# Kernel optimization log

Hardware: AMD Instinct MI355X
Metric: run time of the kernel (lower is better)

The kernel has to match this reference:

```python
import jax, jax.numpy as jnp
import numpy as np

H = 8
D_MODEL = 512
D_K = D_MODEL // H
NEG = -1e9


def setup_inputs() -> dict:
    key = jax.random.key(0)
    ks = jax.random.split(key, 11)
    B, S = 2, 2048
    scale = 1.0 / np.sqrt(D_MODEL)
    inp = {
        'query': jax.random.normal(ks[0], (B, S, D_MODEL), dtype=jnp.float32),
        'key': jax.random.normal(ks[1], (B, S, D_MODEL), dtype=jnp.float32),
        'value': jax.random.normal(ks[2], (B, S, D_MODEL), dtype=jnp.float32),
        'Wq': jax.random.normal(ks[3], (D_MODEL, D_MODEL), dtype=jnp.float32) * scale,
        'bq': jnp.zeros((D_MODEL,), dtype=jnp.float32),
        'Wk': jax.random.normal(ks[4], (D_MODEL, D_MODEL), dtype=jnp.float32) * scale,
        'bk': jnp.zeros((D_MODEL,), dtype=jnp.float32),
        'Wv': jax.random.normal(ks[5], (D_MODEL, D_MODEL), dtype=jnp.float32) * scale,
        'bv': jnp.zeros((D_MODEL,), dtype=jnp.float32),
        'Wo': jax.random.normal(ks[6], (D_MODEL, D_MODEL), dtype=jnp.float32) * scale,
        'bo': jnp.zeros((D_MODEL,), dtype=jnp.float32),
    }
    return inp


def reference(query, key, value, Wq, bq, Wk, bk, Wv, bv, Wo, bo):
    B, S, _ = query.shape
    # QKV projections (nn.Linear: x @ W.T + b), split into heads -> [B, H, S, D_K]
    def proj(x, W, b):
        return (x @ W.T + b).reshape(B, S, H, D_K).transpose(0, 2, 1, 3)

    q = proj(query, Wq, bq)
    k = proj(key, Wk, bk)
    v = proj(value, Wv, bv)

    scores = jnp.einsum('bhqd,bhkd->bhqk', q, k) / jnp.sqrt(jnp.float32(D_K))
    # diagonal mask (mask=True): token cannot attend to itself
    diag = jnp.eye(S, dtype=bool)
    scores = jnp.where(diag, NEG, scores)

    p_attn = jax.nn.softmax(scores, axis=-1)  # [B, H, S, S]
    x = jnp.einsum('bhqk,bhkd->bhqd', p_attn, v)
    x = x.transpose(0, 2, 1, 3).reshape(B, S, H * D_K)
    return x @ Wo.T + bo
```

## Files before the change

### kernel.cpp

```cpp
#include <hip/hip_runtime.h>
#include <hip/hip_bf16.h>
#include <math.h>

#define NUM_H 8
#define DK    64
#define DM    512
#define SEQ   2048
#define NB    2
#define MROWS (NB*SEQ)

typedef unsigned short u16;
typedef unsigned int   u32;
typedef __attribute__((ext_vector_type(8))) __bf16 bf16x8;
typedef __attribute__((ext_vector_type(4))) float  f32x4;

__device__ __forceinline__ u16 f2bf(float v) {
    union { float f; u32 i; } x; x.f = v;
    u32 r = (x.i + 0x7FFFu + ((x.i >> 16) & 1u)) >> 16;
    return (u16)r;
}
__device__ __forceinline__ u16 f2h(float v) {
    union { _Float16 h; u16 u; } x; x.h = (_Float16)v; return x.u;
}
__device__ __forceinline__ float h2f(u16 u) {
    union { u16 u; _Float16 h; } x; x.u = u; return (float)x.h;
}
__device__ __forceinline__ bf16x8 ld_bf8(const u16* p) {
    union { uint4 u; bf16x8 v; } t;
    t.u = *(const uint4*)p;
    return t.v;
}
__device__ __forceinline__ uint4 pack8bf(const float* f) {
    uint4 o;
    o.x = (u32)f2bf(f[0]) | ((u32)f2bf(f[1]) << 16);
    o.y = (u32)f2bf(f[2]) | ((u32)f2bf(f[3]) << 16);
    o.z = (u32)f2bf(f[4]) | ((u32)f2bf(f[5]) << 16);
    o.w = (u32)f2bf(f[6]) | ((u32)f2bf(f[7]) << 16);
    return o;
}

__global__ __launch_bounds__(256) void convAll(
    const float* __restrict__ q, const float* __restrict__ k,
    const float* __restrict__ Wq, const float* __restrict__ Wk,
    const float* __restrict__ Wv, const float* __restrict__ Wo,
    u16* __restrict__ Xqk, u16* __restrict__ Wscr)
{
    const int z = blockIdx.y;
    const float* src;
    u16* dst;
    if (z == 0)      { src = q; dst = Xqk; }
    else if (z == 1) { src = k; dst = Xqk + 2097152; }
    else {
        if (blockIdx.x >= 128) return;
        src = (z == 2) ? Wq : (z == 3) ? Wk : (z == 4) ? Wv : Wo;
        dst = Wscr + (size_t)(z - 2) * 262144;
    }
    int i = (blockIdx.x * 256 + threadIdx.x) * 8;
    float4 a = *(const float4*)(src + i);
    float4 b = *(const float4*)(src + i + 4);
    float f[8] = {a.x, a.y, a.z, a.w, b.x, b.y, b.z, b.w};
    *(uint4*)&dst[i] = pack8bf(f);
}

#define MODE_QK 0
#define MODE_VT 1
#define MODE_FIN 2

template<int MODE, bool INBF, bool WBF>
__device__ __forceinline__ void gemm_core(
    const void* __restrict__ Xv, const void* __restrict__ Wv_,
    const float* __restrict__ bias, void* __restrict__ outv,
    u16* As, u16* Bs, int row0, int col0)
{
    const int tid = threadIdx.x;
    const int lane = tid & 63, w = tid >> 6;
    const int ln15 = lane & 15, quad = lane >> 4;
    const int wm = (w >> 1) * 64, wn = (w & 1) * 32;

    f32x4 acc[4][2];
#pragma unroll
    for (int mt = 0; mt < 4; ++mt)
#pragma unroll
        for (int nt = 0; nt < 2; ++nt) acc[mt][nt] = (f32x4){0.f, 0.f, 0.f, 0.f};

    for (int kt = 0; kt < DM; kt += 64) {
        __syncthreads();
#pragma unroll
        for (int g = 0; g < 4; ++g) {
            int idx = g * 2048 + tid * 8;
            int r = idx >> 6, c = idx & 63;
            if (INBF) {
                *(uint4*)&As[r * 72 + c] =
                    *(const uint4*)((const u16*)Xv + (size_t)(row0 + r) * DM + kt + c);
            } else {
                const float* xp = (const float*)Xv + (size_t)(row0 + r) * DM + kt + c;
                float4 a = *(const float4*)xp;
                float4 b2 = *(const float4*)(xp + 4);
                float f[8] = {a.x, a.y, a.z, a.w, b2.x, b2.y, b2.z, b2.w};
                *(uint4*)&As[r * 72 + c] = pack8bf(f);
            }
        }
#pragma unroll
        for (int g = 0; g < 2; ++g) {
            int idx = g * 2048 + tid * 8;
            int r = idx >> 6, c = idx & 63;
            if (WBF) {
                *(uint4*)&Bs[r * 72 + c] =
                    *(const uint4*)((const u16*)Wv_ + (size_t)(col0 + r) * DM + kt + c);
            } else {
                const float* wp = (const float*)Wv_ + (size_t)(col0 + r) * DM + kt + c;
                float4 a = *(const float4*)wp;
                float4 b2 = *(const float4*)(wp + 4);
                float f[8] = {a.x, a.y, a.z, a.w, b2.x, b2.y, b2.z, b2.w};
                *(uint4*)&Bs[r * 72 + c] = pack8bf(f);
            }
        }
        __syncthreads();

#pragma unroll
        for (int ks = 0; ks < 2; ++ks) {
            bf16x8 af[4], bfr[2];
#pragma unroll
            for (int mt = 0; mt < 4; ++mt)
                af[mt] = ld_bf8(&As[(wm + mt * 16 + ln15) * 72 + ks * 32 + quad * 8]);
#pragma unroll
            for (int nt = 0; nt < 2; ++nt)
                bfr[nt] = ld_bf8(&Bs[(wn + nt * 16 + ln15) * 72 + ks * 32 + quad * 8]);
#pragma unroll
            for (int mt = 0; mt < 4; ++mt)
#pragma unroll
                for (int nt = 0; nt < 2; ++nt)
                    acc[mt][nt] = __builtin_amdgcn_mfma_f32_16x16x32_bf16(
                        af[mt], bfr[nt], acc[mt][nt], 0, 0, 0);
        }
    }

    float bc[2];
#pragma unroll
    for (int nt = 0; nt < 2; ++nt) bc[nt] = bias[col0 + wn + nt * 16 + ln15];
    const int h = col0 >> 6;

    if (MODE == MODE_FIN) {
        float* outF = (float*)outv;
#pragma unroll
        for (int mt = 0; mt < 4; ++mt)
#pragma unroll
            for (int r = 0; r < 4; ++r) {
                int m = row0 + wm + mt * 16 + quad * 4 + r;
#pragma unroll
                for (int nt = 0; nt < 2; ++nt)
                    outF[(size_t)m * DM + col0 + wn + nt * 16 + ln15] = acc[mt][nt][r] + bc[nt];
            }
    } else if (MODE == MODE_QK) {
        u16* outB = (u16*)outv;
#pragma unroll
        for (int mt = 0; mt < 4; ++mt)
#pragma unroll
            for (int r = 0; r < 4; ++r) {
                int m = row0 + wm + mt * 16 + quad * 4 + r;
                int b = m >> 11, s2 = m & (SEQ - 1);
#pragma unroll
                for (int nt = 0; nt < 2; ++nt) {
                    int dk = wn + nt * 16 + ln15;
                    outB[((size_t)((b * NUM_H + h) * SEQ + s2)) * DK + dk] =
                        f2bf(acc[mt][nt][r] + bc[nt]);
                }
            }
    } else {
        u16* outB = (u16*)outv;
        __syncthreads();
#pragma unroll
        for (int mt = 0; mt < 4; ++mt)
#pragma unroll
            for (int nt = 0; nt < 2; ++nt) {
                int dk = wn + nt * 16 + ln15;
#pragma unroll
                for (int r = 0; r < 4; ++r) {
                    int sl = wm + mt * 16 + quad * 4 + r;
                    As[dk * 136 + sl] = f2bf(acc[mt][nt][r] + bc[nt]);
                }
            }
        __syncthreads();
        int dk = tid >> 2, ch = (tid & 3) * 32;
        int b = row0 >> 11, s0 = row0 & (SEQ - 1);
        size_t base = ((size_t)((b * NUM_H + h) * DK + dk)) * SEQ + s0 + ch;
#pragma unroll
        for (int c4 = 0; c4 < 4; ++c4)
            *(uint4*)&outB[base + c4 * 8] = *(const uint4*)&As[dk * 136 + ch + c4 * 8];
    }
}

__global__ __launch_bounds__(256) void qkv_mfma(
    const u16* __restrict__ xq, const u16* __restrict__ xk, const float* __restrict__ xv,
    const u16* __restrict__ Wscr,
    const float* __restrict__ b0, const float* __restrict__ b1, const float* __restrict__ b2,
    u16* __restrict__ oQ, u16* __restrict__ oK, u16* __restrict__ oVt)
{
    __shared__ u16 As[128 * 72];
    __shared__ u16 Bs[64 * 72];
    const int row0 = blockIdx.x * 128, col0 = blockIdx.y * 64;
    const int z = blockIdx.z;
    const u16* W = Wscr + (size_t)z * 262144;
    if (z == 2)
        gemm_core<MODE_VT, false, true>(xv, W, b2, oVt, As, Bs, row0, col0);
    else if (z == 0)
        gemm_core<MODE_QK, true, true>(xq, W, b0, oQ, As, Bs, row0, col0);
    else
        gemm_core<MODE_QK, true, true>(xk, W, b1, oK, As, Bs, row0, col0);
}

__global__ __launch_bounds__(256) void final_mfma(
    const u16* __restrict__ X, const u16* __restrict__ Wbf,
    const float* __restrict__ bias, float* __restrict__ out)
{
    __shared__ u16 As[128 * 72];
    __shared__ u16 Bs[64 * 72];
    gemm_core<MODE_FIN, true, true>(X, Wbf, bias, out, As, Bs,
                                    blockIdx.x * 128, blockIdx.y * 64);
}

#define LSTR 72
__global__ __launch_bounds__(256) void attn_mfma(
    const u16* __restrict__ Qg, const u16* __restrict__ Kg,
    const u16* __restrict__ Vtg, u16* __restrict__ Pd, float* __restrict__ Cl)
{
    __shared__ u16 Klds[64 * LSTR];
    __shared__ u16 Vtlds[64 * LSTR];
    __shared__ u16 Pls[64 * LSTR];

    const int tid = threadIdx.x;
    const int lane = tid & 63;
    const int w = tid >> 6;
    const int ln15 = lane & 15;
    const int quad = lane >> 4;
    const int bh = blockIdx.y;
    const int b = bh >> 3, h = bh & 7;
    const int qb = blockIdx.x * 64;
    const int z = blockIdx.z;
    const int k0 = z * (SEQ / 2), k1 = k0 + SEQ / 2;

    const u16* Qp = Qg + (size_t)bh * SEQ * DK;
    const u16* Kp = Kg + (size_t)bh * SEQ * DK;
    const u16* Vp = Vtg + (size_t)bh * DK * SEQ;

    const int qrowA = qb + w * 16 + ln15;
    const bf16x8 qa0 = ld_bf8(&Qp[(size_t)qrowA * DK + quad * 8]);
    const bf16x8 qa1 = ld_bf8(&Qp[(size_t)qrowA * DK + 32 + quad * 8]);

    f32x4 O[4];
    float l_i[4] = {0.f, 0.f, 0.f, 0.f};
#pragma unroll
    for (int nt = 0; nt < 4; ++nt) O[nt] = (f32x4){0.f, 0.f, 0.f, 0.f};

    const int sr = tid >> 3;
    const int scl = (tid & 7) * 8;

    for (int kt = k0; kt < k1; kt += 64) {
        __syncthreads();
        *(uint4*)&Klds[sr * LSTR + scl]         = *(const uint4*)&Kp[(size_t)(kt + sr) * DK + scl];
        *(uint4*)&Klds[(sr + 32) * LSTR + scl]  = *(const uint4*)&Kp[(size_t)(kt + sr + 32) * DK + scl];
        *(uint4*)&Vtlds[sr * LSTR + scl]        = *(const uint4*)&Vp[(size_t)sr * SEQ + kt + scl];
        *(uint4*)&Vtlds[(sr + 32) * LSTR + scl] = *(const uint4*)&Vp[(size_t)(sr + 32) * SEQ + kt + scl];
        __syncthreads();

        const bool diagt = (kt == qb);
#pragma unroll
        for (int nt2 = 0; nt2 < 4; ++nt2) {
            bf16x8 kb0 = ld_bf8(&Klds[(nt2 * 16 + ln15) * LSTR + quad * 8]);
            bf16x8 kb1 = ld_bf8(&Klds[(nt2 * 16 + ln15) * LSTR + 32 + quad * 8]);
            f32x4 zacc = (f32x4){0.f, 0.f, 0.f, 0.f};
            zacc = __builtin_amdgcn_mfma_f32_16x16x32_bf16(qa0, kb0, zacc, 0, 0, 0);
            zacc = __builtin_amdgcn_mfma_f32_16x16x32_bf16(qa1, kb1, zacc, 0, 0, 0);
#pragma unroll
            for (int r = 0; r < 4; ++r) {
                float e = __expf(fmaf(zacc[r], 0.125f, -4.0f));
                if (diagt && (nt2 * 16 + ln15 == w * 16 + quad * 4 + r)) e = 0.f;
                l_i[r] += e;
                Pls[(w * 16 + quad * 4 + r) * LSTR + nt2 * 16 + ln15] = f2bf(e);
            }
        }

        bf16x8 pa0 = ld_bf8(&Pls[(w * 16 + ln15) * LSTR + quad * 8]);
        bf16x8 pa1 = ld_bf8(&Pls[(w * 16 + ln15) * LSTR + 32 + quad * 8]);
#pragma unroll
        for (int nt = 0; nt < 4; ++nt) {
            bf16x8 vb0 = ld_bf8(&Vtlds[(nt * 16 + ln15) * LSTR + quad * 8]);
            bf16x8 vb1 = ld_bf8(&Vtlds[(nt * 16 + ln15) * LSTR + 32 + quad * 8]);
            O[nt] = __builtin_amdgcn_mfma_f32_16x16x32_bf16(pa0, vb0, O[nt], 0, 0, 0);
            O[nt] = __builtin_amdgcn_mfma_f32_16x16x32_bf16(pa1, vb1, O[nt], 0, 0, 0);
        }
    }

#pragma unroll
    for (int r = 0; r < 4; ++r) {
        float s = l_i[r];
        s += __shfl_xor(s, 1);
        s += __shfl_xor(s, 2);
        s += __shfl_xor(s, 4);
        s += __shfl_xor(s, 8);
        l_i[r] = s;
    }
    if (ln15 == 0) {
#pragma unroll
        for (int r = 0; r < 4; ++r)
            Cl[(size_t)z * 32768 + bh * SEQ + qb + w * 16 + quad * 4 + r] = l_i[r];
    }
#pragma unroll
    for (int r = 0; r < 4; ++r) {
        int s = qb + w * 16 + quad * 4 + r;
        size_t base = (size_t)z * 2097152 + ((size_t)(b * SEQ + s)) * DM + h * DK;
#pragma unroll
        for (int nt = 0; nt < 4; ++nt)
            Pd[base + nt * 16 + ln15] = f2h(O[nt][r] * 0.015625f);
    }
}

__global__ __launch_bounds__(256) void combine(
    const u16* __restrict__ Pd, const float* __restrict__ Cl, u16* __restrict__ C)
{
    int idx = (blockIdx.x * 256 + threadIdx.x) * 8;
    int row = idx >> 9, col = idx & 511;
    int b = row >> 11, s = row & (SEQ - 1), h = col >> 6;
    int bh = b * NUM_H + h;
    float lsum = Cl[bh * SEQ + s] + Cl[32768 + bh * SEQ + s];
    float sc = 64.f / lsum;
    uint4 u0 = *(const uint4*)&Pd[idx];
    uint4 u1 = *(const uint4*)&Pd[2097152 + idx];
    u32 a0[4] = {u0.x, u0.y, u0.z, u0.w};
    u32 a1[4] = {u1.x, u1.y, u1.z, u1.w};
    float f[8];
#pragma unroll
    for (int j = 0; j < 4; ++j) {
        f[2 * j]     = (h2f((u16)(a0[j] & 0xffff)) + h2f((u16)(a1[j] & 0xffff))) * sc;
        f[2 * j + 1] = (h2f((u16)(a0[j] >> 16))    + h2f((u16)(a1[j] >> 16)))    * sc;
    }
    *(uint4*)&C[idx] = pack8bf(f);
}

extern "C" void kernel_launch(void* const* d_in, const int* in_sizes, int n_in,
                              void* d_out, int out_size, void* d_ws, size_t ws_size,
                              hipStream_t stream) {
    const float* q  = (const float*)d_in[0];
    const float* k  = (const float*)d_in[1];
    const float* v  = (const float*)d_in[2];
    const float* Wq = (const float*)d_in[3];
    const float* bq = (const float*)d_in[4];
    const float* Wk = (const float*)d_in[5];
    const float* bk = (const float*)d_in[6];
    const float* Wv = (const float*)d_in[7];
    const float* bv = (const float*)d_in[8];
    const float* Wo = (const float*)d_in[9];
    const float* bo = (const float*)d_in[10];
    float* out = (float*)d_out;

    const size_t TSZ = (size_t)MROWS * DM;
    u16* Qb  = (u16*)d_ws;
    u16* Kb  = Qb + TSZ;
    u16* Vtb = Qb + 2 * TSZ;
    u16* CbU = Qb + 3 * TSZ;
    float* Cl  = (float*)CbU;
    u16*  Wscr = CbU + 131072;

    u16* Xqk = (u16*)d_out;
    u16* Pd  = (u16*)d_out;

    dim3 blk(256);
    hipLaunchKernelGGL(convAll, dim3(1024, 6), blk, 0, stream, q, k, Wq, Wk, Wv, Wo, Xqk, Wscr);
    dim3 gq(MROWS / 128, DM / 64, 3);
    hipLaunchKernelGGL(qkv_mfma, gq, blk, 0, stream,
                       Xqk, Xqk + TSZ, v, Wscr, bq, bk, bv, Qb, Kb, Vtb);
    dim3 ga(SEQ / 64, NB * NUM_H, 2);
    hipLaunchKernelGGL(attn_mfma, ga, blk, 0, stream, Qb, Kb, Vtb, Pd, Cl);
    hipLaunchKernelGGL(combine, dim3(1024), blk, 0, stream, Pd, Cl, Qb);
    dim3 gf(MROWS / 128, DM / 64);
    hipLaunchKernelGGL(final_mfma, gf, blk, 0, stream, Qb, Wscr + 3 * 262144, bo, out);
}
```

Baseline: 174.0 us.

## Double-buffer LDS tiles with register prefetch in GEMM and attention loops

Both the projection GEMM core and the attention kernel now load the next K-tile from global memory into registers while MFMAs run on the current LDS buffer. The prefetched data is then written into a second LDS buffer, which leaves one barrier per iteration instead of two. This is meant to hide global-load latency behind compute. The LDS row stride also drops from 72 to 68 elements, which changes the bank mapping but makes odd rows only 8-byte aligned for 16-byte accesses, so it may cost alignment or bank-conflict penalties. LDS footprint roughly doubles, which may reduce occupancy.

```diff
diff --git a/kernel.cpp b/kernel.cpp
--- a/kernel.cpp
+++ b/kernel.cpp
@@ -13,6 +13,10 @@
 typedef unsigned int   u32;
 typedef __attribute__((ext_vector_type(8))) __bf16 bf16x8;
 typedef __attribute__((ext_vector_type(4))) float  f32x4;
+
+#define ASTR 68
+#define ABUF (128*ASTR)
+#define BBUF (64*ASTR)
 
 __device__ __forceinline__ u16 f2bf(float v) {
     union { float f; u32 i; } x; x.f = v;
@@ -66,9 +70,9 @@
 #define MODE_VT 1
 #define MODE_FIN 2
 
-template<int MODE, bool INBF, bool WBF>
+template<int MODE, bool INBF>
 __device__ __forceinline__ void gemm_core(
-    const void* __restrict__ Xv, const void* __restrict__ Wv_,
+    const void* __restrict__ Xv, const u16* __restrict__ Wb,
     const float* __restrict__ bias, void* __restrict__ outv,
     u16* As, u16* Bs, int row0, int col0)
 {
@@ -77,55 +81,75 @@
     const int ln15 = lane & 15, quad = lane >> 4;
     const int wm = (w >> 1) * 64, wn = (w & 1) * 32;
 
+    const int rA = tid >> 3;
+    const int cA = (tid & 7) * 8;
+
     f32x4 acc[4][2];
 #pragma unroll
     for (int mt = 0; mt < 4; ++mt)
 #pragma unroll
         for (int nt = 0; nt < 2; ++nt) acc[mt][nt] = (f32x4){0.f, 0.f, 0.f, 0.f};
 
-    for (int kt = 0; kt < DM; kt += 64) {
-        __syncthreads();
-#pragma unroll
-        for (int g = 0; g < 4; ++g) {
-            int idx = g * 2048 + tid * 8;
-            int r = idx >> 6, c = idx & 63;
-            if (INBF) {
-                *(uint4*)&As[r * 72 + c] =
-                    *(const uint4*)((const u16*)Xv + (size_t)(row0 + r) * DM + kt + c);
-            } else {
-                const float* xp = (const float*)Xv + (size_t)(row0 + r) * DM + kt + c;
-                float4 a = *(const float4*)xp;
-                float4 b2 = *(const float4*)(xp + 4);
-                float f[8] = {a.x, a.y, a.z, a.w, b2.x, b2.y, b2.z, b2.w};
-                *(uint4*)&As[r * 72 + c] = pack8bf(f);
-            }
-        }
-#pragma unroll
-        for (int g = 0; g < 2; ++g) {
-            int idx = g * 2048 + tid * 8;
-            int r = idx >> 6, c = idx & 63;
-            if (WBF) {
-                *(uint4*)&Bs[r * 72 + c] =
-                    *(const uint4*)((const u16*)Wv_ + (size_t)(col0 + r) * DM + kt + c);
-            } else {
-                const float* wp = (const float*)Wv_ + (size_t)(col0 + r) * DM + kt + c;
-                float4 a = *(const float4*)wp;
-                float4 b2 = *(const float4*)(wp + 4);
-                float f[8] = {a.x, a.y, a.z, a.w, b2.x, b2.y, b2.z, b2.w};
-                *(uint4*)&Bs[r * 72 + c] = pack8bf(f);
-            }
-        }
-        __syncthreads();
-
+    uint4 aU[4];
+    float4 aF0[4], aF1[4];
+    uint4 bU[2];
+
+#pragma unroll
+    for (int g = 0; g < 4; ++g) {
+        int r = row0 + g * 32 + rA;
+        if (INBF) aU[g] = *(const uint4*)((const u16*)Xv + (size_t)r * DM + cA);
+        else {
+            const float* xp = (const float*)Xv + (size_t)r * DM + cA;
+            aF0[g] = *(const float4*)xp; aF1[g] = *(const float4*)(xp + 4);
+        }
+    }
+#pragma unroll
+    for (int g = 0; g < 2; ++g)
+        bU[g] = *(const uint4*)(Wb + (size_t)(col0 + g * 32 + rA) * DM + cA);
+
+#pragma unroll
+    for (int g = 0; g < 4; ++g) {
+        if (!INBF) {
+            float f[8] = {aF0[g].x, aF0[g].y, aF0[g].z, aF0[g].w,
+                          aF1[g].x, aF1[g].y, aF1[g].z, aF1[g].w};
+            aU[g] = pack8bf(f);
+        }
+        *(uint4*)&As[(g * 32 + rA) * ASTR + cA] = aU[g];
+    }
+#pragma unroll
+    for (int g = 0; g < 2; ++g)
+        *(uint4*)&Bs[(g * 32 + rA) * ASTR + cA] = bU[g];
+    __syncthreads();
+
+    int cur = 0;
+    for (int kt_i = 0; kt_i < 8; ++kt_i) {
+        const int ktn = (kt_i + 1) * 64;
+        if (kt_i < 7) {
+#pragma unroll
+            for (int g = 0; g < 4; ++g) {
+                int r = row0 + g * 32 + rA;
+                if (INBF) aU[g] = *(const uint4*)((const u16*)Xv + (size_t)r * DM + ktn + cA);
+                else {
+                    const float* xp = (const float*)Xv + (size_t)r * DM + ktn + cA;
+                    aF0[g] = *(const float4*)xp; aF1[g] = *(const float4*)(xp + 4);
+                }
+            }
+#pragma unroll
+            for (int g = 0; g < 2; ++g)
+                bU[g] = *(const uint4*)(Wb + (size_t)(col0 + g * 32 + rA) * DM + ktn + cA);
+        }
+
+        const u16* Ab = As + cur * ABUF;
+        const u16* Bb = Bs + cur * BBUF;
 #pragma unroll
         for (int ks = 0; ks < 2; ++ks) {
             bf16x8 af[4], bfr[2];
 #pragma unroll
             for (int mt = 0; mt < 4; ++mt)
-                af[mt] = ld_bf8(&As[(wm + mt * 16 + ln15) * 72 + ks * 32 + quad * 8]);
+                af[mt] = ld_bf8(&Ab[(wm + mt * 16 + ln15) * ASTR + ks * 32 + quad * 8]);
 #pragma unroll
             for (int nt = 0; nt < 2; ++nt)
-                bfr[nt] = ld_bf8(&Bs[(wn + nt * 16 + ln15) * 72 + ks * 32 + quad * 8]);
+                bfr[nt] = ld_bf8(&Bb[(wn + nt * 16 + ln15) * ASTR + ks * 32 + quad * 8]);
 #pragma unroll
             for (int mt = 0; mt < 4; ++mt)
 #pragma unroll
@@ -133,6 +157,25 @@
                     acc[mt][nt] = __builtin_amdgcn_mfma_f32_16x16x32_bf16(
                         af[mt], bfr[nt], acc[mt][nt], 0, 0, 0);
         }
+
+        if (kt_i < 7) {
+            u16* An = As + (1 - cur) * ABUF;
+            u16* Bn = Bs + (1 - cur) * BBUF;
+#pragma unroll
+            for (int g = 0; g < 4; ++g) {
+                if (!INBF) {
+                    float f[8] = {aF0[g].x, aF0[g].y, aF0[g].z, aF0[g].w,
+                                  aF1[g].x, aF1[g].y, aF1[g].z, aF1[g].w};
+                    aU[g] = pack8bf(f);
+                }
+                *(uint4*)&An[(g * 32 + rA) * ASTR + cA] = aU[g];
+            }
+#pragma unroll
+            for (int g = 0; g < 2; ++g)
+                *(uint4*)&Bn[(g * 32 + rA) * ASTR + cA] = bU[g];
+        }
+        __syncthreads();
+        cur ^= 1;
     }
 
     float bc[2];
@@ -168,7 +211,6 @@
             }
     } else {
         u16* outB = (u16*)outv;
-        __syncthreads();
 #pragma unroll
         for (int mt = 0; mt < 4; ++mt)
 #pragma unroll
@@ -196,37 +238,36 @@
     const float* __restrict__ b0, const float* __restrict__ b1, const float* __restrict__ b2,
     u16* __restrict__ oQ, u16* __restrict__ oK, u16* __restrict__ oVt)
 {
-    __shared__ u16 As[128 * 72];
-    __shared__ u16 Bs[64 * 72];
+    __shared__ u16 As[2 * ABUF];
+    __shared__ u16 Bs[2 * BBUF];
     const int row0 = blockIdx.x * 128, col0 = blockIdx.y * 64;
     const int z = blockIdx.z;
     const u16* W = Wscr + (size_t)z * 262144;
     if (z == 2)
-        gemm_core<MODE_VT, false, true>(xv, W, b2, oVt, As, Bs, row0, col0);
+        gemm_core<MODE_VT, false>(xv, W, b2, oVt, As, Bs, row0, col0);
     else if (z == 0)
-        gemm_core<MODE_QK, true, true>(xq, W, b0, oQ, As, Bs, row0, col0);
+        gemm_core<MODE_QK, true>(xq, W, b0, oQ, As, Bs, row0, col0);
     else
-        gemm_core<MODE_QK, true, true>(xk, W, b1, oK, As, Bs, row0, col0);
+        gemm_core<MODE_QK, true>(xk, W, b1, oK, As, Bs, row0, col0);
 }
 
 __global__ __launch_bounds__(256) void final_mfma(
     const u16* __restrict__ X, const u16* __restrict__ Wbf,
     const float* __restrict__ bias, float* __restrict__ out)
 {
-    __shared__ u16 As[128 * 72];
-    __shared__ u16 Bs[64 * 72];
-    gemm_core<MODE_FIN, true, true>(X, Wbf, bias, out, As, Bs,
-                                    blockIdx.x * 128, blockIdx.y * 64);
-}
-
-#define LSTR 72
+    __shared__ u16 As[2 * ABUF];
+    __shared__ u16 Bs[2 * BBUF];
+    gemm_core<MODE_FIN, true>(X, Wbf, bias, out, As, Bs,
+                              blockIdx.x * 128, blockIdx.y * 64);
+}
+
 __global__ __launch_bounds__(256) void attn_mfma(
     const u16* __restrict__ Qg, const u16* __restrict__ Kg,
     const u16* __restrict__ Vtg, u16* __restrict__ Pd, float* __restrict__ Cl)
 {
-    __shared__ u16 Klds[64 * LSTR];
-    __shared__ u16 Vtlds[64 * LSTR];
-    __shared__ u16 Pls[64 * LSTR];
+    __shared__ u16 Klds[2 * BBUF];
+    __shared__ u16 Vtlds[2 * BBUF];
+    __shared__ u16 Pls[BBUF];
 
     const int tid = threadIdx.x;
     const int lane = tid & 63;
@@ -255,19 +296,35 @@
     const int sr = tid >> 3;
     const int scl = (tid & 7) * 8;
 
+    uint4 kv0, kv1, vv0, vv1;
+    kv0 = *(const uint4*)&Kp[(size_t)(k0 + sr) * DK + scl];
+    kv1 = *(const uint4*)&Kp[(size_t)(k0 + sr + 32) * DK + scl];
+    vv0 = *(const uint4*)&Vp[(size_t)sr * SEQ + k0 + scl];
+    vv1 = *(const uint4*)&Vp[(size_t)(sr + 32) * SEQ + k0 + scl];
+    *(uint4*)&Klds[sr * ASTR + scl] = kv0;
+    *(uint4*)&Klds[(sr + 32) * ASTR + scl] = kv1;
+    *(uint4*)&Vtlds[sr * ASTR + scl] = vv0;
+    *(uint4*)&Vtlds[(sr + 32) * ASTR + scl] = vv1;
+    __syncthreads();
+
+    int cur = 0;
     for (int kt = k0; kt < k1; kt += 64) {
-        __syncthreads();
-        *(uint4*)&Klds[sr * LSTR + scl]         = *(const uint4*)&Kp[(size_t)(kt + sr) * DK + scl];
-        *(uint4*)&Klds[(sr + 32) * LSTR + scl]  = *(const uint4*)&Kp[(size_t)(kt + sr + 32) * DK + scl];
-        *(uint4*)&Vtlds[sr * LSTR + scl]        = *(const uint4*)&Vp[(size_t)sr * SEQ + kt + scl];
-        *(uint4*)&Vtlds[(sr + 32) * LSTR + scl] = *(const uint4*)&Vp[(size_t)(sr + 32) * SEQ + kt + scl];
-        __syncthreads();
-
+        const int ktn = kt + 64;
+        if (ktn < k1) {
+            kv0 = *(const uint4*)&Kp[(size_t)(ktn + sr) * DK + scl];
+            kv1 = *(const uint4*)&Kp[(size_t)(ktn + sr + 32) * DK + scl];
+            vv0 = *(const uint4*)&Vp[(size_t)sr * SEQ + ktn + scl];
+            vv1 = *(const uint4*)&Vp[(size_t)(sr + 32) * SEQ + ktn + scl];
+        }
+
+        const u16* Kb = Klds + cur * BBUF;
+        const u16* Vb = Vtlds + cur * BBUF;
         const bool diagt = (kt == qb);
+
 #pragma unroll
         for (int nt2 = 0; nt2 < 4; ++nt2) {
-            bf16x8 kb0 = ld_bf8(&Klds[(nt2 * 16 + ln15) * LSTR + quad * 8]);
-            bf16x8 kb1 = ld_bf8(&Klds[(nt2 * 16 + ln15) * LSTR + 32 + quad * 8]);
+            bf16x8 kb0 = ld_bf8(&Kb[(nt2 * 16 + ln15) * ASTR + quad * 8]);
+            bf16x8 kb1 = ld_bf8(&Kb[(nt2 * 16 + ln15) * ASTR + 32 + quad * 8]);
             f32x4 zacc = (f32x4){0.f, 0.f, 0.f, 0.f};
             zacc = __builtin_amdgcn_mfma_f32_16x16x32_bf16(qa0, kb0, zacc, 0, 0, 0);
             zacc = __builtin_amdgcn_mfma_f32_16x16x32_bf16(qa1, kb1, zacc, 0, 0, 0);
@@ -276,19 +333,30 @@
                 float e = __expf(fmaf(zacc[r], 0.125f, -4.0f));
                 if (diagt && (nt2 * 16 + ln15 == w * 16 + quad * 4 + r)) e = 0.f;
                 l_i[r] += e;
-                Pls[(w * 16 + quad * 4 + r) * LSTR + nt2 * 16 + ln15] = f2bf(e);
-            }
-        }
-
-        bf16x8 pa0 = ld_bf8(&Pls[(w * 16 + ln15) * LSTR + quad * 8]);
-        bf16x8 pa1 = ld_bf8(&Pls[(w * 16 + ln15) * LSTR + 32 + quad * 8]);
+                Pls[(w * 16 + quad * 4 + r) * ASTR + nt2 * 16 + ln15] = f2bf(e);
+            }
+        }
+
+        bf16x8 pa0 = ld_bf8(&Pls[(w * 16 + ln15) * ASTR + quad * 8]);
+        bf16x8 pa1 = ld_bf8(&Pls[(w * 16 + ln15) * ASTR + 32 + quad * 8]);
 #pragma unroll
         for (int nt = 0; nt < 4; ++nt) {
-            bf16x8 vb0 = ld_bf8(&Vtlds[(nt * 16 + ln15) * LSTR + quad * 8]);
-            bf16x8 vb1 = ld_bf8(&Vtlds[(nt * 16 + ln15) * LSTR + 32 + quad * 8]);
+            bf16x8 vb0 = ld_bf8(&Vb[(nt * 16 + ln15) * ASTR + quad * 8]);
+            bf16x8 vb1 = ld_bf8(&Vb[(nt * 16 + ln15) * ASTR + 32 + quad * 8]);
             O[nt] = __builtin_amdgcn_mfma_f32_16x16x32_bf16(pa0, vb0, O[nt], 0, 0, 0);
             O[nt] = __builtin_amdgcn_mfma_f32_16x16x32_bf16(pa1, vb1, O[nt], 0, 0, 0);
         }
+
+        if (ktn < k1) {
+            u16* Kn = Klds + (1 - cur) * BBUF;
+            u16* Vn = Vtlds + (1 - cur) * BBUF;
+            *(uint4*)&Kn[sr * ASTR + scl] = kv0;
+            *(uint4*)&Kn[(sr + 32) * ASTR + scl] = kv1;
+            *(uint4*)&Vn[sr * ASTR + scl] = vv0;
+            *(uint4*)&Vn[(sr + 32) * ASTR + scl] = vv1;
+        }
+        __syncthreads();
+        cur ^= 1;
     }
 
 #pragma unroll
```

Result: slower. 311.1 us (+78.8%).
